# Performance work log

Measured on AMD Instinct MI355X. Metric: run time of the kernel, lower is better.

Reference implementation:

```python
import jax, jax.numpy as jnp
import numpy as np

N_NODES = 10000
EPS = 1e-5


def _layernorm(x, gamma, beta):
    mu = jnp.mean(x, axis=-1, keepdims=True)
    var = jnp.mean(jnp.square(x - mu), axis=-1, keepdims=True)
    return (x - mu) * jax.lax.rsqrt(var + EPS) * gamma + beta


def _sage_pool_layer(h, src, dst, Wp, bp, Ws, Wn, b, gamma, beta):
    # DGL SAGEConv(aggregator='pool'):
    #   m_u = relu(h_u @ Wp^T + bp); h_neigh[v] = max_{u in N(v)} m_u (0 if no neighbors)
    #   rst = h @ Ws^T + h_neigh @ Wn^T + b
    m = jax.nn.relu(h @ Wp.T + bp)              # [N, d]
    msg = m[src]                                 # [E, d] gather
    agg = jax.ops.segment_max(msg, dst, num_segments=N_NODES)
    agg = jnp.where(jnp.isfinite(agg), agg, 0.0)  # isolated nodes -> 0
    rst = h @ Ws.T + agg @ Wn.T + b
    # gsage_layer: LayerNorm, then Encoder applies relu (dropout inactive in eval)
    return jax.nn.relu(_layernorm(rst, gamma, beta))


def setup_inputs() -> dict:
    key = jax.random.key(0)
    ks = jax.random.split(key, 16)
    d = 256
    E = 320000
    s = 1.0 / np.sqrt(d)
    inp = {
        "h": jax.random.normal(ks[0], (N_NODES, d), dtype=jnp.float32),
        "edge_src": jax.random.randint(ks[1], (E,), 0, N_NODES, dtype=jnp.int32),
        "edge_dst": jax.random.randint(ks[2], (E,), 0, N_NODES, dtype=jnp.int32),
    }
    for li in range(2):
        kk = jax.random.split(ks[3 + li], 3)
        inp[f"Wp{li}"] = jax.random.normal(kk[0], (d, d), dtype=jnp.float32) * s
        inp[f"bp{li}"] = jnp.zeros((d,), jnp.float32)
        inp[f"Ws{li}"] = jax.random.normal(kk[1], (d, d), dtype=jnp.float32) * s
        inp[f"Wn{li}"] = jax.random.normal(kk[2], (d, d), dtype=jnp.float32) * s
        inp[f"b{li}"] = jnp.zeros((d,), jnp.float32)
        inp[f"g{li}"] = jnp.ones((d,), jnp.float32)
        inp[f"be{li}"] = jnp.zeros((d,), jnp.float32)
    return inp


def reference(h, edge_src, edge_dst,
              Wp0, bp0, Ws0, Wn0, b0, g0, be0,
              Wp1, bp1, Ws1, Wn1, b1, g1, be1):
    h = _sage_pool_layer(h, edge_src, edge_dst, Wp0, bp0, Ws0, Wn0, b0, g0, be0)
    h = _sage_pool_layer(h, edge_src, edge_dst, Wp1, bp1, Ws1, Wn1, b1, g1, be1)
    return h
```

## Files before the change

### kernel.cpp

```cpp
#include <hip/hip_runtime.h>

#define D 256
#define CAP 128
#define ASTRIDE 280
#define LN_EPS 1e-5f

typedef short short8 __attribute__((ext_vector_type(8)));
typedef float floatx4 __attribute__((ext_vector_type(4)));
typedef unsigned short u16x8 __attribute__((ext_vector_type(8)));

__device__ __forceinline__ u16x8 umax8(u16x8 a, u16x8 b) {
#if __has_builtin(__builtin_elementwise_max)
    return __builtin_elementwise_max(a, b);
#else
    u16x8 r;
#pragma unroll
    for (int i = 0; i < 8; i++) r[i] = a[i] > b[i] ? a[i] : b[i];
    return r;
#endif
}

__device__ __forceinline__ unsigned short f2b(float f) {
    union { float f; unsigned int u; } x; x.f = f;
    unsigned int u = x.u + 0x7FFFu + ((x.u >> 16) & 1u);
    return (unsigned short)(u >> 16);
}

#define GEMM_HALF(APTR_EXPR, WPTR, K0H)                                         \
    {                                                                           \
        short8 aF[4], bF[4][4];                                                 \
        _Pragma("unroll") for (int ks = 0; ks < 4; ks++)                        \
            aF[ks] = APTR_EXPR(K0H + ks * 32);                                  \
        _Pragma("unroll") for (int ks = 0; ks < 4; ks++)                        \
        _Pragma("unroll") for (int t = 0; t < 4; t++)                           \
            bF[ks][t] = *(const short8*)((WPTR) + t * 16 * D + (K0H) + ks * 32);\
        _Pragma("unroll") for (int ks = 0; ks < 4; ks++) {                      \
            acc[0] = __builtin_amdgcn_mfma_f32_16x16x32_bf16(aF[ks], bF[ks][0], acc[0], 0, 0, 0); \
            acc[1] = __builtin_amdgcn_mfma_f32_16x16x32_bf16(aF[ks], bF[ks][1], acc[1], 0, 0, 0); \
            acc[2] = __builtin_amdgcn_mfma_f32_16x16x32_bf16(aF[ks], bF[ks][2], acc[2], 0, 0, 0); \
            acc[3] = __builtin_amdgcn_mfma_f32_16x16x32_bf16(aF[ks], bF[ks][3], acc[3], 0, 0, 0); \
        }                                                                       \
    }

__global__ __launch_bounds__(256) void prep_kernel(
    const float* __restrict__ w0, const float* __restrict__ w1,
    const float* __restrict__ w2, const float* __restrict__ w3,
    const float* __restrict__ w4, const float* __restrict__ w5,
    unsigned short* __restrict__ wb,
    const float* __restrict__ h, unsigned short* __restrict__ hb, int nh4,
    int* __restrict__ cnt, unsigned short* __restrict__ mb,
    unsigned short* __restrict__ m1b, int N)
{
    const int blk = blockIdx.x;
    const int tid = threadIdx.x;
    if (blk < 384) {
        const int wsel = blk >> 6;
        const float* src;
        switch (wsel) {
            case 0: src = w0; break; case 1: src = w1; break;
            case 2: src = w2; break; case 3: src = w3; break;
            case 4: src = w4; break; default: src = w5; break;
        }
        const int idx = (blk & 63) * 1024 + tid * 4;
        const float4 v = *(const float4*)(src + idx);
        ushort4 o;
        o.x = f2b(v.x); o.y = f2b(v.y); o.z = f2b(v.z); o.w = f2b(v.w);
        *(ushort4*)(wb + (size_t)wsel * 65536 + idx) = o;
    } else if (blk < 1024) {
        int i = (blk - 384) * 256 + tid;
        const int stride = 640 * 256;
        for (; i < nh4; i += stride) {
            const float4 v = *(const float4*)(h + (size_t)i * 4);
            ushort4 o;
            o.x = f2b(v.x); o.y = f2b(v.y); o.z = f2b(v.z); o.w = f2b(v.w);
            *(ushort4*)(hb + (size_t)i * 4) = o;
        }
    } else if (blk < 1064) {
        const int i = (blk - 1024) * 256 + tid;
        if (i < N) cnt[i] = 0;
    } else {
        mb[(size_t)N * D + tid] = 0;
        m1b[(size_t)N * D + tid] = 0;
    }
}

__global__ __launch_bounds__(64, 4) void gemm_relu(
    const unsigned short* __restrict__ A, const unsigned short* __restrict__ W,
    const float* __restrict__ bias, unsigned short* __restrict__ out_b, int N,
    const int* __restrict__ esrc, const int* __restrict__ edst,
    int* __restrict__ cnt, unsigned short* __restrict__ csr, int E, int ngemm)
{
    if ((int)blockIdx.x >= ngemm) {
        const int nsb = gridDim.x - ngemm;
        int i = ((int)blockIdx.x - ngemm) * 64 + threadIdx.x;
        const int stride = nsb * 64;
        for (; i < E; i += stride) {
            const int d = edst[i];
            const int pos = atomicAdd(&cnt[d], 1);
            if (pos < CAP) csr[(size_t)d * CAP + pos] = (unsigned short)esrc[i];
        }
        return;
    }

    const int lane = threadIdx.x;
    const int quad = lane >> 4;
    const int l16 = lane & 15;
    const int blk = blockIdx.x;
    const int row0 = (blk >> 2) * 16;
    const int col0 = (blk & 3) * 64;
    const int koff = quad * 8;

    floatx4 acc[4];
#pragma unroll
    for (int t = 0; t < 4; t++) acc[t] = (floatx4)(0.f);

    const unsigned short* aptr = A + (size_t)(row0 + l16) * D + koff;
    const unsigned short* wptr = W + (size_t)(col0 + l16) * D + koff;
#define A_GLOBAL(K) (*(const short8*)(aptr + (K)))
    GEMM_HALF(A_GLOBAL, wptr, 0)
    GEMM_HALF(A_GLOBAL, wptr, 128)
#undef A_GLOBAL

#pragma unroll
    for (int t = 0; t < 4; t++) {
        const float bcol = bias[col0 + t * 16 + l16];
#pragma unroll
        for (int r = 0; r < 4; r++) {
            const int rg = row0 + quad * 4 + r;
            const int col = col0 + t * 16 + l16;
            out_b[(size_t)rg * D + col] = f2b(fmaxf(acc[t][r] + bcol, 0.f));
        }
    }
}

__global__ __launch_bounds__(256, 3) void gemm_ln_pool(
    const unsigned short* __restrict__ A, const unsigned short* __restrict__ Wself,
    const unsigned short* __restrict__ Wneigh,
    const unsigned short* __restrict__ mpool,
    const int* __restrict__ cnt, const unsigned short* __restrict__ csr,
    const float* __restrict__ bias,
    const float* __restrict__ gamma, const float* __restrict__ beta,
    unsigned short* __restrict__ out_b, float* __restrict__ out_f,
    const unsigned short* __restrict__ Wnext, const float* __restrict__ bnext,
    unsigned short* __restrict__ mout, int N)
{
    __shared__ unsigned short idxS[16][CAP];
    __shared__ unsigned short aggS[16 * ASTRIDE];
    __shared__ float redS[4][16], redS2[4][16], muA[16], rsA[16];

    const int tid = threadIdx.x;
    const int wave = tid >> 6;
    const int lane = tid & 63;
    const int quad = lane >> 4;
    const int l16 = lane & 15;
    const int row0 = blockIdx.x * 16;
    const int koff = quad * 8;
    const int rbase = wave * 4;
    const int half = lane >> 5;
    const int l32 = lane & 31;

    int degs[4];
#pragma unroll
    for (int rr = 0; rr < 4; rr++) degs[rr] = min(cnt[row0 + rbase + rr], CAP);
    int P = max(max(degs[0], degs[1]), max(degs[2], degs[3]));
    const int P2R = (P + 7) & ~7;
#pragma unroll
    for (int rr = 0; rr < 4; rr++) {
        const int rg = row0 + rbase + rr;
        for (int i = lane; i < P2R; i += 64)
            idxS[rbase + rr][i] = (i < degs[rr]) ? csr[(size_t)rg * CAP + i]
                                                 : (unsigned short)N;
    }

    const int nb = P2R >> 1;
    const unsigned short* mbase = mpool + l32 * 8;

#define ISSUE_B(SL, bi)                                                         \
    {                                                                           \
        _Pragma("unroll") for (int rr = 0; rr < 4; rr++) {                      \
            const int jj = idxS[rbase + rr][2 * (bi) + half];                   \
            SL[rr] = *(const u16x8*)(mbase + (size_t)jj * D);                   \
        }                                                                       \
    }
#define CONS_B(SL)                                                              \
    {                                                                           \
        _Pragma("unroll") for (int rr = 0; rr < 4; rr++)                        \
            mx[rr] = umax8(mx[rr], SL[rr]);                                     \
    }

    u16x8 g0[4], g1[4], g2[4], g3[4];
    u16x8 mx[4];
#pragma unroll
    for (int rr = 0; rr < 4; rr++) mx[rr] = (u16x8)(0);

    if (nb) {
        ISSUE_B(g0, 0) ISSUE_B(g1, 1) ISSUE_B(g2, 2) ISSUE_B(g3, 3)
    }

    floatx4 acc[4];
#pragma unroll
    for (int t = 0; t < 4; t++) acc[t] = (floatx4)(0.f);

    {
        const unsigned short* aptr = A + (size_t)(row0 + l16) * D + koff;
        const unsigned short* wptr = Wself + (size_t)(wave * 64 + l16) * D + koff;
#pragma unroll
        for (int k0 = 0; k0 < D; k0 += 32) {
            const short8 av = *(const short8*)(aptr + k0);
            const short8 b0 = *(const short8*)(wptr + k0);
            const short8 b1 = *(const short8*)(wptr + 16 * D + k0);
            const short8 b2 = *(const short8*)(wptr + 32 * D + k0);
            const short8 b3 = *(const short8*)(wptr + 48 * D + k0);
            acc[0] = __builtin_amdgcn_mfma_f32_16x16x32_bf16(av, b0, acc[0], 0, 0, 0);
            acc[1] = __builtin_amdgcn_mfma_f32_16x16x32_bf16(av, b1, acc[1], 0, 0, 0);
            acc[2] = __builtin_amdgcn_mfma_f32_16x16x32_bf16(av, b2, acc[2], 0, 0, 0);
            acc[3] = __builtin_amdgcn_mfma_f32_16x16x32_bf16(av, b3, acc[3], 0, 0, 0);
        }
    }

    for (int b = 0; b < nb; b += 4) {
        const bool more = (b + 8 <= nb);
        CONS_B(g0) if (more) ISSUE_B(g0, b + 4)
        CONS_B(g1) if (more) ISSUE_B(g1, b + 5)
        CONS_B(g2) if (more) ISSUE_B(g2, b + 6)
        CONS_B(g3) if (more) ISSUE_B(g3, b + 7)
    }
#undef ISSUE_B
#undef CONS_B

#pragma unroll
    for (int rr = 0; rr < 4; rr++) {
        union { u16x8 v; int w[4]; } cur, oth;
        cur.v = mx[rr];
#pragma unroll
        for (int k = 0; k < 4; k++) oth.w[k] = __shfl_xor(cur.w[k], 32);
        const u16x8 mf = umax8(cur.v, oth.v);
        if (half == 0)
            *(u16x8*)&aggS[(rbase + rr) * ASTRIDE + l32 * 8] = mf;
    }
    __syncthreads();

    {
        const unsigned short* wptr = Wneigh + (size_t)(wave * 64 + l16) * D + koff;
#pragma unroll
        for (int k0 = 0; k0 < D; k0 += 32) {
            const short8 av = *(const short8*)&aggS[l16 * ASTRIDE + koff + k0];
            const short8 b0 = *(const short8*)(wptr + k0);
            const short8 b1 = *(const short8*)(wptr + 16 * D + k0);
            const short8 b2 = *(const short8*)(wptr + 32 * D + k0);
            const short8 b3 = *(const short8*)(wptr + 48 * D + k0);
            acc[0] = __builtin_amdgcn_mfma_f32_16x16x32_bf16(av, b0, acc[0], 0, 0, 0);
            acc[1] = __builtin_amdgcn_mfma_f32_16x16x32_bf16(av, b1, acc[1], 0, 0, 0);
            acc[2] = __builtin_amdgcn_mfma_f32_16x16x32_bf16(av, b2, acc[2], 0, 0, 0);
            acc[3] = __builtin_amdgcn_mfma_f32_16x16x32_bf16(av, b3, acc[3], 0, 0, 0);
        }
    }

    float bcol[4];
#pragma unroll
    for (int t = 0; t < 4; t++) bcol[t] = bias[wave * 64 + t * 16 + l16];
#pragma unroll
    for (int t = 0; t < 4; t++)
#pragma unroll
        for (int r = 0; r < 4; r++) acc[t][r] += bcol[t];

#pragma unroll
    for (int r = 0; r < 4; r++) {
        float s = 0.f, s2 = 0.f;
#pragma unroll
        for (int t = 0; t < 4; t++) {
            const float v = acc[t][r];
            s += v; s2 += v * v;
        }
        s += __shfl_xor(s, 1);  s2 += __shfl_xor(s2, 1);
        s += __shfl_xor(s, 2);  s2 += __shfl_xor(s2, 2);
        s += __shfl_xor(s, 4);  s2 += __shfl_xor(s2, 4);
        s += __shfl_xor(s, 8);  s2 += __shfl_xor(s2, 8);
        if (l16 == 0) {
            redS[wave][quad * 4 + r] = s;
            redS2[wave][quad * 4 + r] = s2;
        }
    }
    __syncthreads();
    if (tid < 16) {
        const float S  = redS[0][tid] + redS[1][tid] + redS[2][tid] + redS[3][tid];
        const float S2 = redS2[0][tid] + redS2[1][tid] + redS2[2][tid] + redS2[3][tid];
        const float mu = S * (1.f / D);
        float var = S2 * (1.f / D) - mu * mu;
        var = fmaxf(var, 0.f);
        muA[tid] = mu;
        rsA[tid] = rsqrtf(var + LN_EPS);
    }
    __syncthreads();

    float gcol[4], becol[4];
#pragma unroll
    for (int t = 0; t < 4; t++) {
        gcol[t] = gamma[wave * 64 + t * 16 + l16];
        becol[t] = beta[wave * 64 + t * 16 + l16];
    }
#pragma unroll
    for (int r = 0; r < 4; r++) {
        const int rl = quad * 4 + r;
        const int rg = row0 + rl;
        const float mu = muA[rl];
        const float rs = rsA[rl];
#pragma unroll
        for (int t = 0; t < 4; t++) {
            const int col = wave * 64 + t * 16 + l16;
            float o = (acc[t][r] - mu) * rs * gcol[t] + becol[t];
            o = fmaxf(o, 0.f);
            const unsigned short ob = f2b(o);
            if (out_f) out_f[(size_t)rg * D + col] = o;
            else       out_b[(size_t)rg * D + col] = ob;
            if (Wnext) aggS[rl * ASTRIDE + col] = ob;
        }
    }

    if (Wnext) {
        __syncthreads();
#pragma unroll
        for (int t = 0; t < 4; t++) acc[t] = (floatx4)(0.f);
        const unsigned short* wptr = Wnext + (size_t)(wave * 64 + l16) * D + koff;
#pragma unroll
        for (int k0 = 0; k0 < D; k0 += 32) {
            const short8 av = *(const short8*)&aggS[l16 * ASTRIDE + koff + k0];
            const short8 b0 = *(const short8*)(wptr + k0);
            const short8 b1 = *(const short8*)(wptr + 16 * D + k0);
            const short8 b2 = *(const short8*)(wptr + 32 * D + k0);
            const short8 b3 = *(const short8*)(wptr + 48 * D + k0);
            acc[0] = __builtin_amdgcn_mfma_f32_16x16x32_bf16(av, b0, acc[0], 0, 0, 0);
            acc[1] = __builtin_amdgcn_mfma_f32_16x16x32_bf16(av, b1, acc[1], 0, 0, 0);
            acc[2] = __builtin_amdgcn_mfma_f32_16x16x32_bf16(av, b2, acc[2], 0, 0, 0);
            acc[3] = __builtin_amdgcn_mfma_f32_16x16x32_bf16(av, b3, acc[3], 0, 0, 0);
        }
#pragma unroll
        for (int t = 0; t < 4; t++) {
            const float bc = bnext[wave * 64 + t * 16 + l16];
#pragma unroll
            for (int r = 0; r < 4; r++) {
                const int rg = row0 + quad * 4 + r;
                const int col = wave * 64 + t * 16 + l16;
                mout[(size_t)rg * D + col] = f2b(fmaxf(acc[t][r] + bc, 0.f));
            }
        }
    }
}

extern "C" void kernel_launch(void* const* d_in, const int* in_sizes, int n_in,
                              void* d_out, int out_size, void* d_ws, size_t ws_size,
                              hipStream_t stream) {
    const float* h    = (const float*)d_in[0];
    const int*   esrc = (const int*)d_in[1];
    const int*   edst = (const int*)d_in[2];
    const float* Wp0  = (const float*)d_in[3];
    const float* bp0  = (const float*)d_in[4];
    const float* Ws0  = (const float*)d_in[5];
    const float* Wn0  = (const float*)d_in[6];
    const float* b0   = (const float*)d_in[7];
    const float* g0   = (const float*)d_in[8];
    const float* be0  = (const float*)d_in[9];
    const float* Wp1  = (const float*)d_in[10];
    const float* bp1  = (const float*)d_in[11];
    const float* Ws1  = (const float*)d_in[12];
    const float* Wn1  = (const float*)d_in[13];
    const float* b1   = (const float*)d_in[14];
    const float* g1   = (const float*)d_in[15];
    const float* be1  = (const float*)d_in[16];

    const int N = in_sizes[0] / D;
    const int E = in_sizes[1];
    const size_t ND = (size_t)N * D;

    unsigned short* hb  = (unsigned short*)d_ws;
    unsigned short* mb  = hb + ND;
    unsigned short* h1b = mb + ND + D;
    unsigned short* wb  = h1b + ND;
    int* cnt = (int*)(wb + 6 * 65536);
    unsigned short* csr = (unsigned short*)(cnt + N);
    unsigned short* m1b = csr + (size_t)N * CAP;

    unsigned short* wpb0 = wb + 0 * 65536;
    unsigned short* wsb0 = wb + 1 * 65536;
    unsigned short* wnb0 = wb + 2 * 65536;
    unsigned short* wpb1 = wb + 3 * 65536;
    unsigned short* wsb1 = wb + 4 * 65536;
    unsigned short* wnb1 = wb + 5 * 65536;

    const int rblocks = (N / 16) * 4;
    const int pblocks = N / 16;
    const int sblocks = 1024;

    prep_kernel<<<1065, 256, 0, stream>>>(Wp0, Ws0, Wn0, Wp1, Ws1, Wn1, wb,
                                          h, hb, (int)(ND / 4), cnt, mb, m1b, N);

    gemm_relu<<<rblocks + sblocks, 64, 0, stream>>>(hb, wpb0, bp0, mb, N,
                                                    esrc, edst, cnt, csr, E, rblocks);
    gemm_ln_pool<<<pblocks, 256, 0, stream>>>(hb, wsb0, wnb0, mb, cnt, csr,
                                              b0, g0, be0, h1b, nullptr,
                                              wpb1, bp1, m1b, N);

    gemm_ln_pool<<<pblocks, 256, 0, stream>>>(h1b, wsb1, wnb1, m1b, cnt, csr,
                                              b1, g1, be1, nullptr, (float*)d_out,
                                              nullptr, nullptr, nullptr, N);
}
```

Measured before the change: 216.5 us.

## Fuse h fp32-to-bf16 conversion into first pool GEMM with 4-wave blocks

Moves the h float-to-bf16 conversion out of the prep kernel and into the first pool-projection GEMM. That GEMM now reads fp32 h directly, converts it in registers, and writes the bf16 copy out once from wave 0. The GEMM is also regrouped from one-wave blocks over 64 columns into four-wave blocks over all 256 columns per 16-row tile. This removes one full read and write pass over h in prep, and because each block now loads a row tile only once, A reloads drop. The trade-off is that the fp32 A read is twice as wide and conversion ALU work lands inside the GEMM; the edge-scatter blocks are resized to 256 threads.

```diff
diff --git a/kernel.cpp b/kernel.cpp
--- a/kernel.cpp
+++ b/kernel.cpp
@@ -26,28 +26,11 @@
     return (unsigned short)(u >> 16);
 }
 
-#define GEMM_HALF(APTR_EXPR, WPTR, K0H)                                         \
-    {                                                                           \
-        short8 aF[4], bF[4][4];                                                 \
-        _Pragma("unroll") for (int ks = 0; ks < 4; ks++)                        \
-            aF[ks] = APTR_EXPR(K0H + ks * 32);                                  \
-        _Pragma("unroll") for (int ks = 0; ks < 4; ks++)                        \
-        _Pragma("unroll") for (int t = 0; t < 4; t++)                           \
-            bF[ks][t] = *(const short8*)((WPTR) + t * 16 * D + (K0H) + ks * 32);\
-        _Pragma("unroll") for (int ks = 0; ks < 4; ks++) {                      \
-            acc[0] = __builtin_amdgcn_mfma_f32_16x16x32_bf16(aF[ks], bF[ks][0], acc[0], 0, 0, 0); \
-            acc[1] = __builtin_amdgcn_mfma_f32_16x16x32_bf16(aF[ks], bF[ks][1], acc[1], 0, 0, 0); \
-            acc[2] = __builtin_amdgcn_mfma_f32_16x16x32_bf16(aF[ks], bF[ks][2], acc[2], 0, 0, 0); \
-            acc[3] = __builtin_amdgcn_mfma_f32_16x16x32_bf16(aF[ks], bF[ks][3], acc[3], 0, 0, 0); \
-        }                                                                       \
-    }
-
 __global__ __launch_bounds__(256) void prep_kernel(
     const float* __restrict__ w0, const float* __restrict__ w1,
     const float* __restrict__ w2, const float* __restrict__ w3,
     const float* __restrict__ w4, const float* __restrict__ w5,
     unsigned short* __restrict__ wb,
-    const float* __restrict__ h, unsigned short* __restrict__ hb, int nh4,
     int* __restrict__ cnt, unsigned short* __restrict__ mb,
     unsigned short* __restrict__ m1b, int N)
 {
@@ -66,17 +49,8 @@
         ushort4 o;
         o.x = f2b(v.x); o.y = f2b(v.y); o.z = f2b(v.z); o.w = f2b(v.w);
         *(ushort4*)(wb + (size_t)wsel * 65536 + idx) = o;
-    } else if (blk < 1024) {
-        int i = (blk - 384) * 256 + tid;
-        const int stride = 640 * 256;
-        for (; i < nh4; i += stride) {
-            const float4 v = *(const float4*)(h + (size_t)i * 4);
-            ushort4 o;
-            o.x = f2b(v.x); o.y = f2b(v.y); o.z = f2b(v.z); o.w = f2b(v.w);
-            *(ushort4*)(hb + (size_t)i * 4) = o;
-        }
-    } else if (blk < 1064) {
-        const int i = (blk - 1024) * 256 + tid;
+    } else if (blk < 424) {
+        const int i = (blk - 384) * 256 + tid;
         if (i < N) cnt[i] = 0;
     } else {
         mb[(size_t)N * D + tid] = 0;
@@ -84,16 +58,17 @@
     }
 }
 
-__global__ __launch_bounds__(64, 4) void gemm_relu(
-    const unsigned short* __restrict__ A, const unsigned short* __restrict__ W,
-    const float* __restrict__ bias, unsigned short* __restrict__ out_b, int N,
+__global__ __launch_bounds__(256, 3) void relu_m(
+    const float* __restrict__ h, const unsigned short* __restrict__ Wp,
+    const float* __restrict__ bp, unsigned short* __restrict__ mb,
+    unsigned short* __restrict__ hb, int N,
     const int* __restrict__ esrc, const int* __restrict__ edst,
     int* __restrict__ cnt, unsigned short* __restrict__ csr, int E, int ngemm)
 {
     if ((int)blockIdx.x >= ngemm) {
         const int nsb = gridDim.x - ngemm;
-        int i = ((int)blockIdx.x - ngemm) * 64 + threadIdx.x;
-        const int stride = nsb * 64;
+        int i = ((int)blockIdx.x - ngemm) * 256 + threadIdx.x;
+        const int stride = nsb * 256;
         for (; i < E; i += stride) {
             const int d = edst[i];
             const int pos = atomicAdd(&cnt[d], 1);
@@ -102,33 +77,49 @@
         return;
     }
 
-    const int lane = threadIdx.x;
+    const int tid = threadIdx.x;
+    const int wave = tid >> 6;
+    const int lane = tid & 63;
     const int quad = lane >> 4;
     const int l16 = lane & 15;
-    const int blk = blockIdx.x;
-    const int row0 = (blk >> 2) * 16;
-    const int col0 = (blk & 3) * 64;
+    const int row0 = blockIdx.x * 16;
     const int koff = quad * 8;
 
     floatx4 acc[4];
 #pragma unroll
     for (int t = 0; t < 4; t++) acc[t] = (floatx4)(0.f);
 
-    const unsigned short* aptr = A + (size_t)(row0 + l16) * D + koff;
-    const unsigned short* wptr = W + (size_t)(col0 + l16) * D + koff;
-#define A_GLOBAL(K) (*(const short8*)(aptr + (K)))
-    GEMM_HALF(A_GLOBAL, wptr, 0)
-    GEMM_HALF(A_GLOBAL, wptr, 128)
-#undef A_GLOBAL
+    const float* aptr = h + (size_t)(row0 + l16) * D + koff;
+    const unsigned short* wptr = Wp + (size_t)(wave * 64 + l16) * D + koff;
+#pragma unroll
+    for (int k0 = 0; k0 < D; k0 += 32) {
+        const float4 f0 = *(const float4*)(aptr + k0);
+        const float4 f1 = *(const float4*)(aptr + k0 + 4);
+        union { short8 s; ushort4 h[2]; } av;
+        av.h[0].x = f2b(f0.x); av.h[0].y = f2b(f0.y);
+        av.h[0].z = f2b(f0.z); av.h[0].w = f2b(f0.w);
+        av.h[1].x = f2b(f1.x); av.h[1].y = f2b(f1.y);
+        av.h[1].z = f2b(f1.z); av.h[1].w = f2b(f1.w);
+        if (wave == 0)
+            *(short8*)(hb + (size_t)(row0 + l16) * D + koff + k0) = av.s;
+        const short8 b0 = *(const short8*)(wptr + k0);
+        const short8 b1 = *(const short8*)(wptr + 16 * D + k0);
+        const short8 b2 = *(const short8*)(wptr + 32 * D + k0);
+        const short8 b3 = *(const short8*)(wptr + 48 * D + k0);
+        acc[0] = __builtin_amdgcn_mfma_f32_16x16x32_bf16(av.s, b0, acc[0], 0, 0, 0);
+        acc[1] = __builtin_amdgcn_mfma_f32_16x16x32_bf16(av.s, b1, acc[1], 0, 0, 0);
+        acc[2] = __builtin_amdgcn_mfma_f32_16x16x32_bf16(av.s, b2, acc[2], 0, 0, 0);
+        acc[3] = __builtin_amdgcn_mfma_f32_16x16x32_bf16(av.s, b3, acc[3], 0, 0, 0);
+    }
 
 #pragma unroll
     for (int t = 0; t < 4; t++) {
-        const float bcol = bias[col0 + t * 16 + l16];
+        const float bcol = bp[wave * 64 + t * 16 + l16];
 #pragma unroll
         for (int r = 0; r < 4; r++) {
             const int rg = row0 + quad * 4 + r;
-            const int col = col0 + t * 16 + l16;
-            out_b[(size_t)rg * D + col] = f2b(fmaxf(acc[t][r] + bcol, 0.f));
+            const int col = wave * 64 + t * 16 + l16;
+            mb[(size_t)rg * D + col] = f2b(fmaxf(acc[t][r] + bcol, 0.f));
         }
     }
 }
@@ -188,8 +179,7 @@
             mx[rr] = umax8(mx[rr], SL[rr]);                                     \
     }
 
-    u16x8 g0[4], g1[4], g2[4], g3[4];
-    u16x8 mx[4];
+    u16x8 g0[4], g1[4], g2[4], g3[4], mx[4];
 #pragma unroll
     for (int rr = 0; rr < 4; rr++) mx[rr] = (u16x8)(0);
 
@@ -387,20 +377,19 @@
     unsigned short* wsb1 = wb + 4 * 65536;
     unsigned short* wnb1 = wb + 5 * 65536;
 
-    const int rblocks = (N / 16) * 4;
-    const int pblocks = N / 16;
+    const int gblocks = N / 16;
     const int sblocks = 1024;
 
-    prep_kernel<<<1065, 256, 0, stream>>>(Wp0, Ws0, Wn0, Wp1, Ws1, Wn1, wb,
-                                          h, hb, (int)(ND / 4), cnt, mb, m1b, N);
-
-    gemm_relu<<<rblocks + sblocks, 64, 0, stream>>>(hb, wpb0, bp0, mb, N,
-                                                    esrc, edst, cnt, csr, E, rblocks);
-    gemm_ln_pool<<<pblocks, 256, 0, stream>>>(hb, wsb0, wnb0, mb, cnt, csr,
+    prep_kernel<<<425, 256, 0, stream>>>(Wp0, Ws0, Wn0, Wp1, Ws1, Wn1, wb,
+                                         cnt, mb, m1b, N);
+
+    relu_m<<<gblocks + sblocks, 256, 0, stream>>>(h, wpb0, bp0, mb, hb, N,
+                                                  esrc, edst, cnt, csr, E, gblocks);
+    gemm_ln_pool<<<gblocks, 256, 0, stream>>>(hb, wsb0, wnb0, mb, cnt, csr,
                                               b0, g0, be0, h1b, nullptr,
                                               wpb1, bp1, m1b, N);
 
-    gemm_ln_pool<<<pblocks, 256, 0, stream>>>(h1b, wsb1, wnb1, m1b, cnt, csr,
+    gemm_ln_pool<<<gblocks, 256, 0, stream>>>(h1b, wsb1, wnb1, m1b, cnt, csr,
                                               b1, g1, be1, nullptr, (float*)d_out,
                                               nullptr, nullptr, nullptr, N);
 }
```

Measured after the change: 219.6 us. About the same (+1.4%).
